# Performance work log

Measured on AMD Instinct MI355X. Metric: run time of the kernel, lower is better.

The kernel has to match this reference:

```python
import jax, jax.numpy as jnp
import numpy as np

DIM = 256
NUM_HEADS = 8
HEAD_DIM = DIM // NUM_HEADS  # 32
DILATIONS = (1, 2, 4, 8)
ND = len(DILATIONS)          # 4
K = 3                        # kernel_size
KK = K * K                   # 9
SCALE = HEAD_DIM ** -0.5
LN_EPS = 1e-5


def _unfold(t, dil, k=K):
    # t: (B, d, H, W) -> (B, d, k*k, H, W); same-size dilated im2col (stride 1,
    # padding dil*(k-1)//2), kernel positions in row-major order like nn.Unfold.
    B, d, H, W = t.shape
    p = dil * (k - 1) // 2
    tp = jnp.pad(t, ((0, 0), (0, 0), (p, p), (p, p)))
    patches = [tp[:, :, i * dil:i * dil + H, j * dil:j * dil + W]
               for i in range(k) for j in range(k)]
    return jnp.stack(patches, axis=2)


def setup_inputs() -> dict:
    key = jax.random.key(0)
    ks = jax.random.split(key, 10)
    B, C, H, W = 8, DIM, 64, 64
    s = lambda fan: fan ** -0.5
    return {
        "x": jax.random.normal(ks[0], (B, C, H, W), jnp.float32),
        "qkv_w": jax.random.normal(ks[1], (3 * C, C), jnp.float32) * s(C),
        "qkv_b": jnp.zeros((3 * C,), jnp.float32),
        "fc_w": jax.random.normal(ks[2], (ND, ND), jnp.float32) * s(ND),
        "fc_b": jnp.zeros((ND,), jnp.float32),
        "ln_g": jnp.ones((C // ND,), jnp.float32),
        "ln_b": jnp.zeros((C // ND,), jnp.float32),
        "proj_w": jax.random.normal(ks[3], (C, C), jnp.float32) * s(C),
        "proj_b": jnp.zeros((C,), jnp.float32),
    }


def reference(x, qkv_w, qkv_b, fc_w, fc_b, ln_g, ln_b, proj_w, proj_b):
    B, C, H, W = x.shape
    d = C // ND            # channels per dilation branch
    h = d // HEAD_DIM      # heads per branch
    L = H * W

    # 1x1 conv qkv: (B, 3C, H, W) -> (B, 3, ND, d, H, W)
    qkv = jnp.einsum('bchw,oc->bohw', x, qkv_w) + qkv_b[None, :, None, None]
    qkv = qkv.reshape(B, 3, ND, d, H, W)

    feats = []
    for i, dil in enumerate(DILATIONS):
        q = qkv[:, 0, i]                                # (B, d, H, W)
        kmap = qkv[:, 1, i]
        vmap = qkv[:, 2, i]
        qr = q.reshape(B, h, HEAD_DIM, L)               # (B, h, hd, L)
        ku = _unfold(kmap, dil).reshape(B, h, HEAD_DIM, KK, L)
        vu = _unfold(vmap, dil).reshape(B, h, HEAD_DIM, KK, L)
        # per-pixel window attention: scores (B, h, L, KK)
        attn = jnp.einsum('bhcl,bhcpl->bhlp', qr, ku) * SCALE
        attn = jax.nn.softmax(attn, axis=-1)
        out = jnp.einsum('bhlp,bhcpl->bhlc', attn, vu)  # (B, h, L, hd)
        feats.append(out.transpose(0, 2, 1, 3).reshape(B, H, W, d))

    # Cross-scale fusion: mix the S=ND scale axis with a small linear layer
    stacked = jnp.stack(feats, axis=3)                  # (B, H, W, S, d)
    fused = jnp.einsum('bhwsc,ts->bhwtc', stacked, fc_w) \
        + fc_b[None, None, None, :, None]
    fused = fused + stacked
    mu = fused.mean(axis=-1, keepdims=True)
    var = fused.var(axis=-1, keepdims=True)
    fused = (fused - mu) * jax.lax.rsqrt(var + LN_EPS) * ln_g + ln_b

    y2 = fused.reshape(B, H, W, C)
    y3 = y2 @ proj_w.T + proj_b
    return y3.transpose(0, 3, 1, 2)                     # (B, C, H, W)
```

## Files before the change

### kernel.cpp

```cpp
#include <hip/hip_runtime.h>
#include <stdint.h>

typedef __attribute__((ext_vector_type(8))) short bf16x8;
typedef __attribute__((ext_vector_type(4))) float f32x4;

#define AS1 __attribute__((address_space(1)))
#define AS3 __attribute__((address_space(3)))

__device__ __forceinline__ void gload_lds16(const void* g, void* l){
  __builtin_amdgcn_global_load_lds((AS1 void*)g, (AS3 void*)l, 16, 0, 0);
}

__device__ __forceinline__ unsigned short to_bf16(float f){
  union { float f; unsigned int i; } x; x.f = f;
  unsigned int u = x.i;
  unsigned int r = (u + 0x7fffu + ((u >> 16) & 1u)) >> 16;
  return (unsigned short)r;
}
__device__ __forceinline__ float bf2f(unsigned short s){
  union { unsigned int i; float f; } x; x.i = ((unsigned int)s) << 16; return x.f;
}
__device__ __forceinline__ float bflo(unsigned int u){
  union { unsigned int i; float f; } x; x.i = u << 16; return x.f;
}
__device__ __forceinline__ float bfhi(unsigned int u){
  union { unsigned int i; float f; } x; x.i = u & 0xffff0000u; return x.f;
}
__device__ __forceinline__ void unp8(uint4 v, float* f){
  f[0]=bflo(v.x); f[1]=bfhi(v.x); f[2]=bflo(v.y); f[3]=bfhi(v.y);
  f[4]=bflo(v.z); f[5]=bfhi(v.z); f[6]=bflo(v.w); f[7]=bfhi(v.w);
}

__global__ __launch_bounds__(256) void prep_kernel(const float* __restrict__ x,
                                                   unsigned short* __restrict__ xb,
                                                   const float* __restrict__ qkv_w,
                                                   const float* __restrict__ proj_w,
                                                   unsigned short* __restrict__ wq,
                                                   unsigned short* __restrict__ wp){
  int bid = blockIdx.x;
  int tid = threadIdx.x;
  if (bid >= 2048){
    int i = (bid - 2048) * 256 + tid;
    const int nq4 = 768 * 256 / 4;
    const int np4 = 256 * 256 / 4;
    if (i < nq4){
      float4 v = ((const float4*)qkv_w)[i];
      ushort4 u; u.x = to_bf16(v.x); u.y = to_bf16(v.y); u.z = to_bf16(v.z); u.w = to_bf16(v.w);
      ((ushort4*)wq)[i] = u;
    } else if (i < nq4 + np4){
      float4 v = ((const float4*)proj_w)[i - nq4];
      ushort4 u; u.x = to_bf16(v.x); u.y = to_bf16(v.y); u.z = to_bf16(v.z); u.w = to_bf16(v.w);
      ((ushort4*)wp)[i - nq4] = u;
    }
    return;
  }
  __shared__ float tile[64][65];
  int l0 = (bid & 63) * 64;
  int c0 = ((bid >> 6) & 3) * 64;
  int b  = bid >> 8;
  const float* xp = x + ((size_t)b * 256 + c0) * 4096 + l0;
  #pragma unroll
  for (int rep = 0; rep < 4; rep++){
    int idx = rep * 256 + tid;
    int cl = idx >> 4, q4 = idx & 15;
    float4 v = *(const float4*)(xp + (size_t)cl * 4096 + q4 * 4);
    tile[cl][q4 * 4 + 0] = v.x;
    tile[cl][q4 * 4 + 1] = v.y;
    tile[cl][q4 * 4 + 2] = v.z;
    tile[cl][q4 * 4 + 3] = v.w;
  }
  __syncthreads();
  unsigned short* op = xb + ((size_t)b * 4096 + l0) * 256 + c0;
  #pragma unroll
  for (int rep = 0; rep < 4; rep++){
    int idx = rep * 256 + tid;
    int ll = idx >> 4, cp = (idx & 15) * 4;
    ushort4 u;
    u.x = to_bf16(tile[cp + 0][ll]);
    u.y = to_bf16(tile[cp + 1][ll]);
    u.z = to_bf16(tile[cp + 2][ll]);
    u.w = to_bf16(tile[cp + 3][ll]);
    *(ushort4*)(op + (size_t)ll * 256 + cp) = u;
  }
}

__device__ __forceinline__ void stage_tile(const unsigned short* __restrict__ A,
                                           const unsigned short* __restrict__ B,
                                           unsigned short* la, unsigned short* lb,
                                           int tid, int wave, int k0){
  #pragma unroll
  for (int inst = 0; inst < 4; inst++){
    int u    = inst * 256 + tid;
    int row  = u >> 3;
    int col  = u & 7;
    int scol = col ^ (row & 7);
    gload_lds16(A + (size_t)row * 256 + k0 + scol * 8, la + inst * 2048 + wave * 512);
    gload_lds16(B + (size_t)row * 256 + k0 + scol * 8, lb + inst * 2048 + wave * 512);
  }
}

__device__ __forceinline__ void compute_tile(const unsigned short* la, const unsigned short* lb,
                                             int lane, int m_w, int n_w, f32x4 acc[4][4]){
  #pragma unroll
  for (int kk = 0; kk < 2; kk++){
    bf16x8 ar[4], br[4];
    int slot = kk * 4 + (lane >> 4);
    #pragma unroll
    for (int i = 0; i < 4; i++){
      int rowa = m_w + i * 16 + (lane & 15);
      ar[i] = *(const bf16x8*)((const char*)la + rowa * 128 + ((slot ^ (rowa & 7)) << 4));
      int rowb = n_w + i * 16 + (lane & 15);
      br[i] = *(const bf16x8*)((const char*)lb + rowb * 128 + ((slot ^ (rowb & 7)) << 4));
    }
    #pragma unroll
    for (int i = 0; i < 4; i++){
      #pragma unroll
      for (int j = 0; j < 4; j++)
        acc[i][j] = __builtin_amdgcn_mfma_f32_16x16x32_bf16(ar[i], br[j], acc[i][j], 0, 0, 0);
    }
  }
}

__global__ __launch_bounds__(256, 2) void qkv_gemm_kernel(
    const unsigned short* __restrict__ Wq, const unsigned short* __restrict__ xb,
    const float* __restrict__ qkv_b, unsigned short* __restrict__ qkv){
  __shared__ __align__(16) unsigned short lA[2][128 * 64];
  __shared__ __align__(16) unsigned short lB[2][128 * 64];
  int orig   = blockIdx.x;
  int b      = orig & 7;
  int tile   = orig >> 3;
  int tile_m = tile % 6;
  int tile_n = tile / 6;
  int tid  = threadIdx.x;
  int lane = tid & 63;
  int wave = tid >> 6;
  int m_w = (wave >> 1) * 64;
  int n_w = (wave & 1) * 64;

  f32x4 zero; zero[0]=0.f; zero[1]=0.f; zero[2]=0.f; zero[3]=0.f;
  f32x4 acc[4][4];
  #pragma unroll
  for (int i = 0; i < 4; i++)
    #pragma unroll
    for (int j = 0; j < 4; j++) acc[i][j] = zero;

  const unsigned short* Abase = Wq + (size_t)tile_m * 128 * 256;
  const unsigned short* Bbase = xb + ((size_t)b * 4096 + (size_t)tile_n * 128) * 256;

  stage_tile(Abase, Bbase, lA[0], lB[0], tid, wave, 0);
  __syncthreads();
  #pragma unroll
  for (int ks = 0; ks < 4; ks++){
    int cur = ks & 1, nxt = cur ^ 1;
    if (ks < 3) stage_tile(Abase, Bbase, lA[nxt], lB[nxt], tid, wave, (ks + 1) * 64);
    compute_tile(lA[cur], lB[cur], lane, m_w, n_w, acc);
    if (ks < 3) __syncthreads();
  }

  #pragma unroll
  for (int i = 0; i < 4; i++){
    #pragma unroll
    for (int j = 0; j < 4; j++){
      int l  = tile_n * 128 + n_w + j * 16 + (lane & 15);
      int o0 = tile_m * 128 + m_w + i * 16 + ((lane >> 4) << 2);
      ushort4 u;
      u.x = to_bf16(acc[i][j][0] + qkv_b[o0 + 0]);
      u.y = to_bf16(acc[i][j][1] + qkv_b[o0 + 1]);
      u.z = to_bf16(acc[i][j][2] + qkv_b[o0 + 2]);
      u.w = to_bf16(acc[i][j][3] + qkv_b[o0 + 3]);
      *(ushort4*)(qkv + ((size_t)(b * 24 + (o0 >> 5)) * 4096 + l) * 32 + (o0 & 31)) = u;
    }
  }
}

__global__ __launch_bounds__(256) void attn_fcln_kernel(
    const unsigned short* __restrict__ qkv,
    const float* __restrict__ fc_w, const float* __restrict__ fc_b,
    const float* __restrict__ ln_g, const float* __restrict__ ln_b,
    unsigned short* __restrict__ y2){
  __shared__ float fsm[16 * 260];
  int tid  = threadIdx.x;
  int orig = blockIdx.x;
  int b    = orig & 7;
  int l0   = (orig >> 3) * 16;
  int lc   = tid & 3;
  int px   = (tid >> 2) & 15;
  int di   = tid >> 6;
  int dil  = 1 << di;
  int l    = l0 + px;
  int yy = l >> 6, xx = l & 63;

  #pragma unroll
  for (int head = 0; head < 2; head++){
    const unsigned short* qp = qkv + ((size_t)(b * 24 +      di * 2 + head) * 4096 + l) * 32 + lc * 8;
    const unsigned short* kb = qkv + ((size_t)(b * 24 +  8 + di * 2 + head) * 4096) * 32;
    const unsigned short* vb = qkv + ((size_t)(b * 24 + 16 + di * 2 + head) * 4096) * 32;
    float qf[8];
    unp8(*(const uint4*)qp, qf);

    float sc[9]; int nidx[9]; bool ib[9];
    #pragma unroll
    for (int p = 0; p < 9; p++){
      int ny = yy + (p / 3 - 1) * dil;
      int nx = xx + (p % 3 - 1) * dil;
      bool in = ((unsigned)ny < 64u) && ((unsigned)nx < 64u);
      ib[p] = in; nidx[p] = ny * 64 + nx;
      float part = 0.f;
      if (in){
        float kf[8];
        unp8(*(const uint4*)(kb + (size_t)nidx[p] * 32 + lc * 8), kf);
        #pragma unroll
        for (int c = 0; c < 8; c++) part += qf[c] * kf[c];
      }
      part += __shfl_xor(part, 1);
      part += __shfl_xor(part, 2);
      sc[p] = part * 0.17677669529663687f;
    }
    float mx = sc[0];
    #pragma unroll
    for (int p = 1; p < 9; p++) mx = fmaxf(mx, sc[p]);
    float w[9]; float den = 0.f;
    #pragma unroll
    for (int p = 0; p < 9; p++){ w[p] = __expf(sc[p] - mx); den += w[p]; }
    float inv = 1.f / den;

    float o[8];
    #pragma unroll
    for (int c = 0; c < 8; c++) o[c] = 0.f;
    #pragma unroll
    for (int p = 0; p < 9; p++){
      if (ib[p]){
        float wp = w[p] * inv;
        float vf[8];
        unp8(*(const uint4*)(vb + (size_t)nidx[p] * 32 + lc * 8), vf);
        #pragma unroll
        for (int c = 0; c < 8; c++) o[c] += wp * vf[c];
      }
    }
    float* fp = fsm + px * 260 + di * 64 + head * 32 + lc * 8;
    #pragma unroll
    for (int c = 0; c < 8; c++) fp[c] = o[c];
  }
  __syncthreads();

  int c = tid & 63;
  int w = tid >> 6;
  float g  = ln_g[c], bb = ln_b[c];
  float fw[4][4], fb[4];
  #pragma unroll
  for (int t = 0; t < 4; t++){
    fb[t] = fc_b[t];
    #pragma unroll
    for (int s = 0; s < 4; s++) fw[t][s] = fc_w[t * 4 + s];
  }
  #pragma unroll
  for (int pp = 0; pp < 4; pp++){
    int p = w * 4 + pp;
    float st[4];
    #pragma unroll
    for (int s = 0; s < 4; s++) st[s] = fsm[p * 260 + s * 64 + c];
    unsigned short* op = y2 + ((size_t)(b * 4096) + l0 + p) * 256;
    #pragma unroll
    for (int t = 0; t < 4; t++){
      float v = fb[t] + st[t];
      #pragma unroll
      for (int s = 0; s < 4; s++) v += fw[t][s] * st[s];
      float s1 = v, s2 = v * v;
      #pragma unroll
      for (int m = 1; m < 64; m <<= 1){ s1 += __shfl_xor(s1, m); s2 += __shfl_xor(s2, m); }
      float mu  = s1 * 0.015625f;
      float var = s2 * 0.015625f - mu * mu;
      float rs  = rsqrtf(var + 1e-5f);
      op[t * 64 + c] = to_bf16((v - mu) * rs * g + bb);
    }
  }
}

__global__ __launch_bounds__(256, 2) void proj_gemm_kernel(
    const unsigned short* __restrict__ Wp, const unsigned short* __restrict__ y2,
    const float* __restrict__ proj_b, float* __restrict__ out){
  __shared__ __align__(16) unsigned short lA[2][128 * 64];
  __shared__ __align__(16) unsigned short lB[2][128 * 64];
  int orig   = blockIdx.x;
  int b      = orig & 7;
  int tile   = orig >> 3;
  int tile_m = tile & 1;
  int tile_n = tile >> 1;
  int tid  = threadIdx.x;
  int lane = tid & 63;
  int wave = tid >> 6;
  int m_w = (wave >> 1) * 64;
  int n_w = (wave & 1) * 64;

  f32x4 zero; zero[0]=0.f; zero[1]=0.f; zero[2]=0.f; zero[3]=0.f;
  f32x4 acc[4][4];
  #pragma unroll
  for (int i = 0; i < 4; i++)
    #pragma unroll
    for (int j = 0; j < 4; j++) acc[i][j] = zero;

  const unsigned short* Abase = Wp + (size_t)tile_m * 128 * 256;
  const unsigned short* Bbase = y2 + ((size_t)b * 4096 + (size_t)tile_n * 128) * 256;

  stage_tile(Abase, Bbase, lA[0], lB[0], tid, wave, 0);
  __syncthreads();
  #pragma unroll
  for (int ks = 0; ks < 4; ks++){
    int cur = ks & 1, nxt = cur ^ 1;
    if (ks < 3) stage_tile(Abase, Bbase, lA[nxt], lB[nxt], tid, wave, (ks + 1) * 64);
    compute_tile(lA[cur], lB[cur], lane, m_w, n_w, acc);
    if (ks < 3) __syncthreads();
  }

  #pragma unroll
  for (int i = 0; i < 4; i++){
    #pragma unroll
    for (int j = 0; j < 4; j++){
      int l = tile_n * 128 + n_w + j * 16 + (lane & 15);
      #pragma unroll
      for (int r = 0; r < 4; r++){
        int o = tile_m * 128 + m_w + i * 16 + ((lane >> 4) << 2) + r;
        out[((size_t)b * 256 + o) * 4096 + l] = acc[i][j][r] + proj_b[o];
      }
    }
  }
}

extern "C" void kernel_launch(void* const* d_in, const int* in_sizes, int n_in,
                              void* d_out, int out_size, void* d_ws, size_t ws_size,
                              hipStream_t stream){
  const float* x      = (const float*)d_in[0];
  const float* qkv_w  = (const float*)d_in[1];
  const float* qkv_b  = (const float*)d_in[2];
  const float* fc_w   = (const float*)d_in[3];
  const float* fc_b   = (const float*)d_in[4];
  const float* ln_g   = (const float*)d_in[5];
  const float* ln_b   = (const float*)d_in[6];
  const float* proj_w = (const float*)d_in[7];
  const float* proj_b = (const float*)d_in[8];
  float* out = (float*)d_out;

  unsigned short* xb  = (unsigned short*)d_ws;
  unsigned short* qkv = xb  + (size_t)8 * 4096 * 256;
  unsigned short* wq  = qkv + (size_t)8 * 24 * 4096 * 32;
  unsigned short* wp  = wq  + (size_t)768 * 256;
  unsigned short* y2  = xb;

  hipLaunchKernelGGL(prep_kernel,      dim3(2304), dim3(256), 0, stream, x, xb, qkv_w, proj_w, wq, wp);
  hipLaunchKernelGGL(qkv_gemm_kernel,  dim3(1536), dim3(256), 0, stream, wq, xb, qkv_b, qkv);
  hipLaunchKernelGGL(attn_fcln_kernel, dim3(2048), dim3(256), 0, stream, qkv, fc_w, fc_b, ln_g, ln_b, y2);
  hipLaunchKernelGGL(proj_gemm_kernel, dim3(512),  dim3(256), 0, stream, wp, y2, proj_b, out);
}
```

Baseline: 82.49 us.

## Split attention and fc+LN kernels, stage K/V rows in LDS per image row

The fused attention+fc+LayerNorm kernel is split in two. The new attention kernel gives each block one image row and one dilation, and loads the three needed K and V neighbour rows into LDS with direct global-to-LDS loads, so the 9-tap gathers read from LDS instead of global memory. Results are written as bf16 to an intermediate buffer, and a separate kernel applies the scale-mixing fc and LayerNorm. This trades an extra kernel launch and an extra global round trip of the stacked features, plus bf16 rounding of the intermediate, for better K/V reuse and more coalesced access.

New measurement: 88.60 us. +7.4%, slower.

```diff
diff --git a/kernel.cpp b/kernel.cpp
--- a/kernel.cpp
+++ b/kernel.cpp
@@ -173,42 +173,58 @@
   }
 }
 
-__global__ __launch_bounds__(256) void attn_fcln_kernel(
-    const unsigned short* __restrict__ qkv,
-    const float* __restrict__ fc_w, const float* __restrict__ fc_b,
-    const float* __restrict__ ln_g, const float* __restrict__ ln_b,
-    unsigned short* __restrict__ y2){
-  __shared__ float fsm[16 * 260];
+__global__ __launch_bounds__(256) void attn_kernel(
+    const unsigned short* __restrict__ qkv, unsigned short* __restrict__ stk){
+  __shared__ __align__(16) unsigned short lk[3 * 2 * 64 * 32];
+  __shared__ __align__(16) unsigned short lv[3 * 2 * 64 * 32];
   int tid  = threadIdx.x;
+  int wave = tid >> 6;
   int orig = blockIdx.x;
   int b    = orig & 7;
-  int l0   = (orig >> 3) * 16;
+  int rest = orig >> 3;
+  int di   = rest & 3;
+  int yy   = rest >> 2;
+  int dil  = 1 << di;
   int lc   = tid & 3;
-  int px   = (tid >> 2) & 15;
-  int di   = tid >> 6;
-  int dil  = 1 << di;
-  int l    = l0 + px;
-  int yy = l >> 6, xx = l & 63;
+  int px   = tid >> 2;
+  int l    = yy * 64 + px;
+  int xx   = px;
+
+  bool rv[3];
+  #pragma unroll
+  for (int r = 0; r < 3; r++){
+    int ry = yy + (r - 1) * dil;
+    rv[r] = ((unsigned)ry < 64u);
+    if (rv[r]){
+      #pragma unroll
+      for (int head = 0; head < 2; head++){
+        const unsigned short* ks = qkv + ((size_t)(b * 24 +  8 + di * 2 + head) * 4096 + ry * 64) * 32;
+        const unsigned short* vs = qkv + ((size_t)(b * 24 + 16 + di * 2 + head) * 4096 + ry * 64) * 32;
+        gload_lds16(ks + (size_t)tid * 8, lk + (size_t)(r * 2 + head) * 2048 + wave * 512);
+        gload_lds16(vs + (size_t)tid * 8, lv + (size_t)(r * 2 + head) * 2048 + wave * 512);
+      }
+    }
+  }
+  __syncthreads();
 
   #pragma unroll
   for (int head = 0; head < 2; head++){
-    const unsigned short* qp = qkv + ((size_t)(b * 24 +      di * 2 + head) * 4096 + l) * 32 + lc * 8;
-    const unsigned short* kb = qkv + ((size_t)(b * 24 +  8 + di * 2 + head) * 4096) * 32;
-    const unsigned short* vb = qkv + ((size_t)(b * 24 + 16 + di * 2 + head) * 4096) * 32;
+    const unsigned short* qp = qkv + ((size_t)(b * 24 + di * 2 + head) * 4096 + l) * 32 + lc * 8;
     float qf[8];
     unp8(*(const uint4*)qp, qf);
 
-    float sc[9]; int nidx[9]; bool ib[9];
+    float sc[9]; int lidx[9]; bool ib[9];
     #pragma unroll
     for (int p = 0; p < 9; p++){
-      int ny = yy + (p / 3 - 1) * dil;
+      int r  = p / 3;
       int nx = xx + (p % 3 - 1) * dil;
-      bool in = ((unsigned)ny < 64u) && ((unsigned)nx < 64u);
-      ib[p] = in; nidx[p] = ny * 64 + nx;
+      bool in = rv[r] && ((unsigned)nx < 64u);
+      ib[p] = in;
+      lidx[p] = ((r * 2 + head) * 64 + nx) * 32;
       float part = 0.f;
       if (in){
         float kf[8];
-        unp8(*(const uint4*)(kb + (size_t)nidx[p] * 32 + lc * 8), kf);
+        unp8(*(const uint4*)(lk + lidx[p] + lc * 8), kf);
         #pragma unroll
         for (int c = 0; c < 8; c++) part += qf[c] * kf[c];
       }
@@ -232,47 +248,53 @@
       if (ib[p]){
         float wp = w[p] * inv;
         float vf[8];
-        unp8(*(const uint4*)(vb + (size_t)nidx[p] * 32 + lc * 8), vf);
+        unp8(*(const uint4*)(lv + lidx[p] + lc * 8), vf);
         #pragma unroll
         for (int c = 0; c < 8; c++) o[c] += wp * vf[c];
       }
     }
-    float* fp = fsm + px * 260 + di * 64 + head * 32 + lc * 8;
-    #pragma unroll
-    for (int c = 0; c < 8; c++) fp[c] = o[c];
-  }
-  __syncthreads();
-
-  int c = tid & 63;
-  int w = tid >> 6;
-  float g  = ln_g[c], bb = ln_b[c];
-  float fw[4][4], fb[4];
+    unsigned short* op = stk + ((size_t)(b * 4096 + l) * 4 + di) * 64 + head * 32 + lc * 8;
+    uint4 u;
+    u.x = (unsigned)to_bf16(o[0]) | ((unsigned)to_bf16(o[1]) << 16);
+    u.y = (unsigned)to_bf16(o[2]) | ((unsigned)to_bf16(o[3]) << 16);
+    u.z = (unsigned)to_bf16(o[4]) | ((unsigned)to_bf16(o[5]) << 16);
+    u.w = (unsigned)to_bf16(o[6]) | ((unsigned)to_bf16(o[7]) << 16);
+    *(uint4*)op = u;
+  }
+}
+
+__global__ __launch_bounds__(256) void fcln_kernel(
+    const unsigned short* __restrict__ stk,
+    const float* __restrict__ fc_w, const float* __restrict__ fc_b,
+    const float* __restrict__ ln_g, const float* __restrict__ ln_b,
+    unsigned short* __restrict__ y2){
+  int tid = threadIdx.x;
+  int pix = blockIdx.x * 4 + (tid >> 6);
+  int c   = tid & 63;
+  const unsigned short* sp = stk + (size_t)pix * 256;
+  float st[4];
+  #pragma unroll
+  for (int s = 0; s < 4; s++) st[s] = bf2f(sp[s * 64 + c]);
+  float fused[4];
   #pragma unroll
   for (int t = 0; t < 4; t++){
-    fb[t] = fc_b[t];
-    #pragma unroll
-    for (int s = 0; s < 4; s++) fw[t][s] = fc_w[t * 4 + s];
-  }
-  #pragma unroll
-  for (int pp = 0; pp < 4; pp++){
-    int p = w * 4 + pp;
-    float st[4];
-    #pragma unroll
-    for (int s = 0; s < 4; s++) st[s] = fsm[p * 260 + s * 64 + c];
-    unsigned short* op = y2 + ((size_t)(b * 4096) + l0 + p) * 256;
-    #pragma unroll
-    for (int t = 0; t < 4; t++){
-      float v = fb[t] + st[t];
-      #pragma unroll
-      for (int s = 0; s < 4; s++) v += fw[t][s] * st[s];
-      float s1 = v, s2 = v * v;
-      #pragma unroll
-      for (int m = 1; m < 64; m <<= 1){ s1 += __shfl_xor(s1, m); s2 += __shfl_xor(s2, m); }
-      float mu  = s1 * 0.015625f;
-      float var = s2 * 0.015625f - mu * mu;
-      float rs  = rsqrtf(var + 1e-5f);
-      op[t * 64 + c] = to_bf16((v - mu) * rs * g + bb);
-    }
+    float f = fc_b[t] + st[t];
+    #pragma unroll
+    for (int s = 0; s < 4; s++) f += fc_w[t * 4 + s] * st[s];
+    fused[t] = f;
+  }
+  float g = ln_g[c], bb = ln_b[c];
+  unsigned short* op = y2 + (size_t)pix * 256;
+  #pragma unroll
+  for (int t = 0; t < 4; t++){
+    float v = fused[t];
+    float s1 = v, s2 = v * v;
+    #pragma unroll
+    for (int m = 1; m < 64; m <<= 1){ s1 += __shfl_xor(s1, m); s2 += __shfl_xor(s2, m); }
+    float mu  = s1 * 0.015625f;
+    float var = s2 * 0.015625f - mu * mu;
+    float rs  = rsqrtf(var + 1e-5f);
+    op[t * 64 + c] = to_bf16((v - mu) * rs * g + bb);
   }
 }
 
@@ -342,12 +364,14 @@
 
   unsigned short* xb  = (unsigned short*)d_ws;
   unsigned short* qkv = xb  + (size_t)8 * 4096 * 256;
-  unsigned short* wq  = qkv + (size_t)8 * 24 * 4096 * 32;
+  unsigned short* stk = qkv + (size_t)8 * 24 * 4096 * 32;
+  unsigned short* wq  = stk + (size_t)8 * 4096 * 256;
   unsigned short* wp  = wq  + (size_t)768 * 256;
   unsigned short* y2  = xb;
 
   hipLaunchKernelGGL(prep_kernel,      dim3(2304), dim3(256), 0, stream, x, xb, qkv_w, proj_w, wq, wp);
   hipLaunchKernelGGL(qkv_gemm_kernel,  dim3(1536), dim3(256), 0, stream, wq, xb, qkv_b, qkv);
-  hipLaunchKernelGGL(attn_fcln_kernel, dim3(2048), dim3(256), 0, stream, qkv, fc_w, fc_b, ln_g, ln_b, y2);
+  hipLaunchKernelGGL(attn_kernel,      dim3(2048), dim3(256), 0, stream, qkv, stk);
+  hipLaunchKernelGGL(fcln_kernel,      dim3(8192), dim3(256), 0, stream, stk, fc_w, fc_b, ln_g, ln_b, y2);
   hipLaunchKernelGGL(proj_gemm_kernel, dim3(512),  dim3(256), 0, stream, wp, y2, proj_b, out);
 }
```
